# Kernel tuning notes

Hardware: AMD Instinct MI355X
Metric: run time of the kernel (lower is better)

Reference implementation:

```python
import jax, jax.numpy as jnp
import numpy as np

NUM_NODES = 100000
NUM_NEIGHS = 64
FEAT = 128
BATCH = 16384
NUM_SAMPLES = 16


def setup_inputs() -> dict:
    key = jax.random.key(0)
    k_ids, k_feat, k_adj = jax.random.split(key, 3)
    ids = jax.random.randint(k_ids, (BATCH,), 0, NUM_NODES, dtype=jnp.int64 if jax.config.jax_enable_x64 else jnp.int32)
    features = jax.random.normal(k_feat, (NUM_NODES, FEAT), dtype=jnp.float32)
    adj_info = jax.random.randint(k_adj, (NUM_NODES, NUM_NEIGHS), 0, NUM_NODES, dtype=jnp.int32)
    return {
        "ids": ids,
        "num_samples": NUM_SAMPLES,
        "features": features,
        "batch_size": BATCH,
        "adj_info": adj_info,
    }


def reference(ids, num_samples, features, batch_size, adj_info):
    # Gather adjacency rows and center-node features
    adj_lists = jnp.take(adj_info, ids, axis=0)            # [B, K]
    node_features = jnp.take(features, ids, axis=0)        # [B, F]
    neighbor_feature = jnp.take(features, adj_lists, axis=0)  # [B, K, F]
    # Euclidean distance center -> each neighbor (broadcast instead of tile)
    diff = node_features[:, None, :] - neighbor_feature    # [B, K, F]
    distance = jnp.sqrt(jnp.sum(diff * diff, axis=-1))     # [B, K]
    prob = jnp.exp(-distance)
    prob = prob / jnp.sum(prob, axis=-1, keepdims=True)    # [B, K]
    # Categorical sampling of num_samples neighbors per row
    logits = jnp.log(prob)
    skey = jax.random.key(42)
    samples_idx = jax.random.categorical(skey, logits, axis=-1, shape=(num_samples, batch_size)).T  # [B, S]
    selected = jnp.take_along_axis(adj_lists, samples_idx, axis=1)  # [B, S]
    return selected
```

## Files before the change

kernel.cpp:

```cpp
#include <hip/hip_runtime.h>
#include <stdint.h>

#define NB 16384
#define NK 64
#define NF 128
#define NS 16
#define RPB 4

__device__ __forceinline__ float xla_exp_f32(float x_in) {
#pragma clang fp contract(off)
  const float exp_hi = 88.3762626647950f;
  const float exp_lo = -88.3762626647949f;
  const float log2ef = 1.44269504088896341f;
  const float c1 = 0.693359375f;
  const float c2 = -2.12194440e-4f;
  const float p0 = 1.9875691500E-4f;
  const float p1 = 1.3981999507E-3f;
  const float p2 = 8.3334519073E-3f;
  const float p3 = 4.1665795894E-2f;
  const float p4 = 1.6666665459E-1f;
  const float p5 = 5.0000001201E-1f;

  float x = fminf(fmaxf(x_in, exp_lo), exp_hi);
  float fx = floorf(fmaf(x, log2ef, 0.5f));
  float tmp = c1 * fx;
  float z2 = c2 * fx;
  x = x - tmp;
  x = x - z2;
  float z = x * x;
  float y = fmaf(x, p0, p1);
  y = fmaf(y, x, p2);
  y = fmaf(y, x, p3);
  y = fmaf(y, x, p4);
  y = fmaf(y, x, p5);
  y = fmaf(y, z, x);
  y = y + 1.0f;
  int n = (int)fx;
  float two_n = __int_as_float((n + 127) << 23);
  return fmaxf(y * two_n, x_in);
}

__device__ __forceinline__ float xla_log_f32(float x_in) {
#pragma clang fp contract(off)
  const float sqrthf = 0.707106781186547524f;
  const float p0 = 7.0376836292E-2f;
  const float p1 = -1.1514610310E-1f;
  const float p2 = 1.1676998740E-1f;
  const float p3 = -1.2420140846E-1f;
  const float p4 = 1.4249322787E-1f;
  const float p5 = -1.6668057665E-1f;
  const float p6 = 2.0000714765E-1f;
  const float p7 = -2.4999993993E-1f;
  const float p8 = 3.3333331174E-1f;
  const float q1 = -2.12194440e-4f;
  const float q2 = 0.693359375f;

  float t = fmaxf(x_in, __uint_as_float(0x00800000u));
  uint32_t bits = __float_as_uint(t);
  float e = (float)((int)(bits >> 23) - 0x7f) + 1.0f;
  float m = __uint_as_float((bits & 0x007fffffu) | 0x3f000000u);
  bool lt = (m < sqrthf);
  float madd = lt ? m : 0.0f;
  e = e - (lt ? 1.0f : 0.0f);
  m = (m + madd) - 1.0f;

  float z = m * m;
  float y = fmaf(m, p0, p1);
  y = fmaf(y, m, p2);
  y = fmaf(y, m, p3);
  y = fmaf(y, m, p4);
  y = fmaf(y, m, p5);
  y = fmaf(y, m, p6);
  y = fmaf(y, m, p7);
  y = fmaf(y, m, p8);
  y = y * m;
  y = y * z;
  y = fmaf(e, q1, y);
  y = y - 0.5f * z;
  float r = m + y;
  r = fmaf(e, q2, r);
  return r;
}

__device__ __forceinline__ void threefry2x32_k42(uint32_t c0, uint32_t c1,
                                                 uint32_t& o0, uint32_t& o1) {
  const uint32_t k0 = 0u, k1 = 42u;
  const uint32_t k2 = k0 ^ k1 ^ 0x1BD11BDAu;
  uint32_t x0 = c0 + k0, x1 = c1 + k1;
#define TF_R(r) { x0 += x1; x1 = (x1 << (r)) | (x1 >> (32 - (r))); x1 ^= x0; }
  TF_R(13) TF_R(15) TF_R(26) TF_R(6)
  x0 += k1; x1 += k2 + 1u;
  TF_R(17) TF_R(29) TF_R(16) TF_R(24)
  x0 += k2; x1 += k0 + 2u;
  TF_R(13) TF_R(15) TF_R(26) TF_R(6)
  x0 += k0; x1 += k1 + 3u;
  TF_R(17) TF_R(29) TF_R(16) TF_R(24)
  x0 += k1; x1 += k2 + 4u;
  TF_R(13) TF_R(15) TF_R(26) TF_R(6)
  x0 += k2; x1 += k0 + 5u;
#undef TF_R
  o0 = x0; o1 = x1;
}

__device__ __forceinline__ uint32_t jax_random_bits32(uint32_t m) {
  uint32_t a, b;
  threefry2x32_k42(0u, m, a, b);
  return a ^ b;
}

__device__ __forceinline__ float gumbel_from_bits(uint32_t bits) {
#pragma clang fp contract(off)
  const float tiny = 1.17549435e-38f;
  float f = __uint_as_float((bits >> 9) | 0x3f800000u) - 1.0f;
  float u = fmaxf(tiny, f + tiny);
  return -xla_log_f32(-xla_log_f32(u));
}

#define AS1 __attribute__((address_space(1)))
#define AS3 __attribute__((address_space(3)))

__global__ void __launch_bounds__(256)
dns_kernel(const int* __restrict__ ids, const float* __restrict__ features,
           const int* __restrict__ adj, int* __restrict__ out) {
#pragma clang fp contract(off)
  __shared__ __align__(16) char sbuf[RPB][8192];
  __shared__ __align__(16) float fc[RPB][NF];
  __shared__ __align__(16) float esh[RPB][NK];
  __shared__ int nsh[RPB][NK];
  __shared__ float zb[RPB][NS][4];
  __shared__ int ib[RPB][NS][4];

  const int wave = threadIdx.x >> 6;
  const int k = threadIdx.x & 63;
  const int b = blockIdx.x * RPB + wave;
  char* sb = sbuf[wave];

  float pg[16];
#define GUM1(ss) pg[ss] = gumbel_from_bits(                                  \
      jax_random_bits32((uint32_t)(((ss) * NB + b) * NK + k)))

  const int center = ids[b];
  GUM1(0); GUM1(1); GUM1(2);

  if (k < NF / 4)
    ((float4*)fc[wave])[k] = ((const float4*)(features + (size_t)center * NF))[k];
  nsh[wave][k] = adj[(size_t)center * NK + k];

  GUM1(3); GUM1(4); GUM1(5);
  asm volatile("s_waitcnt lgkmcnt(0)" ::: "memory");

  const int rg = k >> 3;
  const int eg = k & 7;
  const int es = eg ^ rg;

  const float4* f4b = (const float4*)features;
#define MKGP(i) const float4* gp##i = f4b + (size_t)nsh[wave][(i) * 8 + rg] * (NF / 4) + es
  MKGP(0); MKGP(1); MKGP(2); MKGP(3); MKGP(4); MKGP(5); MKGP(6); MKGP(7);
#undef MKGP

#define STAGEQ()                                                             \
  do {                                                                       \
    __builtin_amdgcn_global_load_lds((const AS1 void*)gp0,                   \
        (AS3 void*)(sb + 0 * 1024), 16, 0, 0);                               \
    __builtin_amdgcn_global_load_lds((const AS1 void*)gp1,                   \
        (AS3 void*)(sb + 1 * 1024), 16, 0, 0);                               \
    __builtin_amdgcn_global_load_lds((const AS1 void*)gp2,                   \
        (AS3 void*)(sb + 2 * 1024), 16, 0, 0);                               \
    __builtin_amdgcn_global_load_lds((const AS1 void*)gp3,                   \
        (AS3 void*)(sb + 3 * 1024), 16, 0, 0);                               \
    __builtin_amdgcn_global_load_lds((const AS1 void*)gp4,                   \
        (AS3 void*)(sb + 4 * 1024), 16, 0, 0);                               \
    __builtin_amdgcn_global_load_lds((const AS1 void*)gp5,                   \
        (AS3 void*)(sb + 5 * 1024), 16, 0, 0);                               \
    __builtin_amdgcn_global_load_lds((const AS1 void*)gp6,                   \
        (AS3 void*)(sb + 6 * 1024), 16, 0, 0);                               \
    __builtin_amdgcn_global_load_lds((const AS1 void*)gp7,                   \
        (AS3 void*)(sb + 7 * 1024), 16, 0, 0);                               \
    gp0 += 8; gp1 += 8; gp2 += 8; gp3 += 8;                                  \
    gp4 += 8; gp5 += 8; gp6 += 8; gp7 += 8;                                  \
  } while (0)

#define CONSUMEQ(q)                                                          \
  do {                                                                       \
    _Pragma("unroll")                                                        \
    for (int j2 = 0; j2 < 8; ++j2) {                                         \
      const float4 v =                                                       \
          *(const float4*)(sb + k * 128 + ((j2 ^ (k & 7)) << 4));            \
      const int j = (q) * 8 + j2;                                            \
      float d0 = fc[wave][4 * j + 0] - v.x; acc = acc + d0 * d0;             \
      float d1 = fc[wave][4 * j + 1] - v.y; acc = acc + d1 * d1;             \
      float d2 = fc[wave][4 * j + 2] - v.z; acc = acc + d2 * d2;             \
      float d3 = fc[wave][4 * j + 3] - v.w; acc = acc + d3 * d3;             \
    }                                                                        \
  } while (0)

  float acc = 0.0f;

  STAGEQ(); GUM1(6); GUM1(7); GUM1(8);
  asm volatile("s_waitcnt vmcnt(0)" ::: "memory");
  CONSUMEQ(0);
  asm volatile("s_waitcnt lgkmcnt(0)" ::: "memory");

  STAGEQ(); GUM1(9); GUM1(10); GUM1(11);
  asm volatile("s_waitcnt vmcnt(0)" ::: "memory");
  CONSUMEQ(1);
  asm volatile("s_waitcnt lgkmcnt(0)" ::: "memory");

  STAGEQ(); GUM1(12); GUM1(13);
  asm volatile("s_waitcnt vmcnt(0)" ::: "memory");
  CONSUMEQ(2);
  asm volatile("s_waitcnt lgkmcnt(0)" ::: "memory");

  STAGEQ(); GUM1(14); GUM1(15);
  asm volatile("s_waitcnt vmcnt(0)" ::: "memory");
  CONSUMEQ(3);
  asm volatile("s_waitcnt lgkmcnt(0)" ::: "memory");

  const float ev = xla_exp_f32(-sqrtf(acc));
  esh[wave][k] = ev;
  asm volatile("s_waitcnt lgkmcnt(0)" ::: "memory");

  float s = 0.0f;
  const float4* e4 = (const float4*)esh[wave];
#pragma unroll
  for (int i = 0; i < NK / 4; ++i) {
    float4 v = e4[i];
    s = s + v.x; s = s + v.y; s = s + v.z; s = s + v.w;
  }
  const float logit = xla_log_f32(ev / s);

  float (*zsh)[NK + 1] = (float (*)[NK + 1])(void*)sb;
#pragma unroll
  for (int ss = 0; ss < NS; ++ss) {
    zsh[ss][k] = pg[ss] + logit;
  }
  asm volatile("s_waitcnt lgkmcnt(0)" ::: "memory");

  const int samp = k >> 2;
  const int sub = k & 3;
  const int kbase = sub * 16;
  float best = zsh[samp][kbase];
  int bi = kbase;
#pragma unroll 1
  for (int j = 1; j < 16; ++j) {
    const float v = zsh[samp][kbase + j];
    if (v > best) { best = v; bi = kbase + j; }
  }
  zb[wave][samp][sub] = best;
  ib[wave][samp][sub] = bi;
  asm volatile("s_waitcnt lgkmcnt(0)" ::: "memory");

  if (sub == 0) {
    float bb = zb[wave][samp][0];
    int bbi = ib[wave][samp][0];
#pragma unroll
    for (int qq = 1; qq < 4; ++qq) {
      const float v = zb[wave][samp][qq];
      if (v > bb) { bb = v; bbi = ib[wave][samp][qq]; }
    }
    out[b * NS + samp] = nsh[wave][bbi];
  }
#undef STAGEQ
#undef CONSUMEQ
#undef GUM1
}

extern "C" void kernel_launch(void* const* d_in, const int* in_sizes, int n_in,
                              void* d_out, int out_size, void* d_ws, size_t ws_size,
                              hipStream_t stream) {
  const int* ids = (const int*)d_in[0];
  const float* features = (const float*)d_in[2];
  const int* adj = (const int*)d_in[4];
  int* out = (int*)d_out;
  (void)in_sizes; (void)n_in; (void)out_size; (void)d_ws; (void)ws_size;

  dns_kernel<<<dim3(NB / RPB), dim3(64 * RPB), 0, stream>>>(ids, features, adj, out);
}
```

Before: 81.80 us.

## Split neighbor row loads between LDS staging and direct register loads to shrink LDS

Each lane now fetches half of each 32-float chunk of its own neighbor's feature row straight into registers. The other half still goes through global_load_lds staging into a smaller, re-swizzled LDS buffer. This cuts per-wave LDS from 8KB to 4.5KB, and launch bounds are raised to request 6 blocks per SM, so more waves can hide the gather latency. The cost is more register pressure from the held float4 values, and the direct loads are uncoalesced per-lane row accesses.

```diff
diff --git a/kernel.cpp b/kernel.cpp
--- a/kernel.cpp
+++ b/kernel.cpp
@@ -119,11 +119,11 @@
 #define AS1 __attribute__((address_space(1)))
 #define AS3 __attribute__((address_space(3)))
 
-__global__ void __launch_bounds__(256)
+__global__ void __launch_bounds__(256, 6)
 dns_kernel(const int* __restrict__ ids, const float* __restrict__ features,
            const int* __restrict__ adj, int* __restrict__ out) {
 #pragma clang fp contract(off)
-  __shared__ __align__(16) char sbuf[RPB][8192];
+  __shared__ __align__(16) char sbuf[RPB][4608];
   __shared__ __align__(16) float fc[RPB][NF];
   __shared__ __align__(16) float esh[RPB][NK];
   __shared__ int nsh[RPB][NK];
@@ -142,79 +142,83 @@
   const int center = ids[b];
   GUM1(0); GUM1(1); GUM1(2);
 
+  const int rn = adj[(size_t)center * NK + k];
+  nsh[wave][k] = rn;
   if (k < NF / 4)
     ((float4*)fc[wave])[k] = ((const float4*)(features + (size_t)center * NF))[k];
-  nsh[wave][k] = adj[(size_t)center * NK + k];
 
   GUM1(3); GUM1(4); GUM1(5);
   asm volatile("s_waitcnt lgkmcnt(0)" ::: "memory");
 
-  const int rg = k >> 3;
-  const int eg = k & 7;
-  const int es = eg ^ rg;
-
+  const int rsub = k >> 2;
+  const int gsw = (k & 3) ^ (rsub & 3);
   const float4* f4b = (const float4*)features;
-#define MKGP(i) const float4* gp##i = f4b + (size_t)nsh[wave][(i) * 8 + rg] * (NF / 4) + es
-  MKGP(0); MKGP(1); MKGP(2); MKGP(3); MKGP(4); MKGP(5); MKGP(6); MKGP(7);
-#undef MKGP
-
-#define STAGEQ()                                                             \
-  do {                                                                       \
-    __builtin_amdgcn_global_load_lds((const AS1 void*)gp0,                   \
+  const float4* gp0 = f4b + (size_t)nsh[wave][0 * 16 + rsub] * (NF / 4) + gsw;
+  const float4* gp1 = f4b + (size_t)nsh[wave][1 * 16 + rsub] * (NF / 4) + gsw;
+  const float4* gp2 = f4b + (size_t)nsh[wave][2 * 16 + rsub] * (NF / 4) + gsw;
+  const float4* gp3 = f4b + (size_t)nsh[wave][3 * 16 + rsub] * (NF / 4) + gsw;
+  const float4* gbase = f4b + (size_t)rn * (NF / 4);
+
+  const int csw = k & 3;
+  const char* crow = sb + k * 64;
+  const float4* fc4 = (const float4*)fc[wave];
+  float acc = 0.0f;
+
+#define STAGE_L(L)                                                           \
+    __builtin_amdgcn_global_load_lds((const AS1 void*)(gp0 + (L) * 8),       \
         (AS3 void*)(sb + 0 * 1024), 16, 0, 0);                               \
-    __builtin_amdgcn_global_load_lds((const AS1 void*)gp1,                   \
+    __builtin_amdgcn_global_load_lds((const AS1 void*)(gp1 + (L) * 8),       \
         (AS3 void*)(sb + 1 * 1024), 16, 0, 0);                               \
-    __builtin_amdgcn_global_load_lds((const AS1 void*)gp2,                   \
+    __builtin_amdgcn_global_load_lds((const AS1 void*)(gp2 + (L) * 8),       \
         (AS3 void*)(sb + 2 * 1024), 16, 0, 0);                               \
-    __builtin_amdgcn_global_load_lds((const AS1 void*)gp3,                   \
+    __builtin_amdgcn_global_load_lds((const AS1 void*)(gp3 + (L) * 8),       \
         (AS3 void*)(sb + 3 * 1024), 16, 0, 0);                               \
-    __builtin_amdgcn_global_load_lds((const AS1 void*)gp4,                   \
-        (AS3 void*)(sb + 4 * 1024), 16, 0, 0);                               \
-    __builtin_amdgcn_global_load_lds((const AS1 void*)gp5,                   \
-        (AS3 void*)(sb + 5 * 1024), 16, 0, 0);                               \
-    __builtin_amdgcn_global_load_lds((const AS1 void*)gp6,                   \
-        (AS3 void*)(sb + 6 * 1024), 16, 0, 0);                               \
-    __builtin_amdgcn_global_load_lds((const AS1 void*)gp7,                   \
-        (AS3 void*)(sb + 7 * 1024), 16, 0, 0);                               \
-    gp0 += 8; gp1 += 8; gp2 += 8; gp3 += 8;                                  \
-    gp4 += 8; gp5 += 8; gp6 += 8; gp7 += 8;                                  \
-  } while (0)
-
-#define CONSUMEQ(q)                                                          \
-  do {                                                                       \
+    const float4 sc0_##L = gbase[(L) * 8 + 4];                               \
+    const float4 sc1_##L = gbase[(L) * 8 + 5];                               \
+    const float4 sc2_##L = gbase[(L) * 8 + 6];                               \
+    const float4 sc3_##L = gbase[(L) * 8 + 7]
+
+#define DQ(f, v)                                                             \
+    { float d0 = (f).x - (v).x; acc = acc + d0 * d0;                         \
+      float d1 = (f).y - (v).y; acc = acc + d1 * d1;                         \
+      float d2 = (f).z - (v).z; acc = acc + d2 * d2;                         \
+      float d3 = (f).w - (v).w; acc = acc + d3 * d3; }
+
+#define CONSUME_L(L)                                                         \
     _Pragma("unroll")                                                        \
-    for (int j2 = 0; j2 < 8; ++j2) {                                         \
-      const float4 v =                                                       \
-          *(const float4*)(sb + k * 128 + ((j2 ^ (k & 7)) << 4));            \
-      const int j = (q) * 8 + j2;                                            \
-      float d0 = fc[wave][4 * j + 0] - v.x; acc = acc + d0 * d0;             \
-      float d1 = fc[wave][4 * j + 1] - v.y; acc = acc + d1 * d1;             \
-      float d2 = fc[wave][4 * j + 2] - v.z; acc = acc + d2 * d2;             \
-      float d3 = fc[wave][4 * j + 3] - v.w; acc = acc + d3 * d3;             \
+    for (int t = 0; t < 4; ++t) {                                            \
+      const float4 v = *(const float4*)(crow + ((t ^ csw) << 4));            \
+      DQ(fc4[(L) * 8 + t], v);                                               \
     }                                                                        \
-  } while (0)
-
-  float acc = 0.0f;
-
-  STAGEQ(); GUM1(6); GUM1(7); GUM1(8);
-  asm volatile("s_waitcnt vmcnt(0)" ::: "memory");
-  CONSUMEQ(0);
-  asm volatile("s_waitcnt lgkmcnt(0)" ::: "memory");
-
-  STAGEQ(); GUM1(9); GUM1(10); GUM1(11);
-  asm volatile("s_waitcnt vmcnt(0)" ::: "memory");
-  CONSUMEQ(1);
-  asm volatile("s_waitcnt lgkmcnt(0)" ::: "memory");
-
-  STAGEQ(); GUM1(12); GUM1(13);
-  asm volatile("s_waitcnt vmcnt(0)" ::: "memory");
-  CONSUMEQ(2);
-  asm volatile("s_waitcnt lgkmcnt(0)" ::: "memory");
-
-  STAGEQ(); GUM1(14); GUM1(15);
-  asm volatile("s_waitcnt vmcnt(0)" ::: "memory");
-  CONSUMEQ(3);
-  asm volatile("s_waitcnt lgkmcnt(0)" ::: "memory");
+    DQ(fc4[(L) * 8 + 4], sc0_##L);                                           \
+    DQ(fc4[(L) * 8 + 5], sc1_##L);                                           \
+    DQ(fc4[(L) * 8 + 6], sc2_##L);                                           \
+    DQ(fc4[(L) * 8 + 7], sc3_##L)
+
+  {
+    STAGE_L(0); GUM1(6); GUM1(7); GUM1(8);
+    asm volatile("s_waitcnt vmcnt(0)" ::: "memory");
+    CONSUME_L(0);
+    asm volatile("s_waitcnt lgkmcnt(0)" ::: "memory");
+  }
+  {
+    STAGE_L(1); GUM1(9); GUM1(10); GUM1(11);
+    asm volatile("s_waitcnt vmcnt(0)" ::: "memory");
+    CONSUME_L(1);
+    asm volatile("s_waitcnt lgkmcnt(0)" ::: "memory");
+  }
+  {
+    STAGE_L(2); GUM1(12); GUM1(13);
+    asm volatile("s_waitcnt vmcnt(0)" ::: "memory");
+    CONSUME_L(2);
+    asm volatile("s_waitcnt lgkmcnt(0)" ::: "memory");
+  }
+  {
+    STAGE_L(3); GUM1(14); GUM1(15);
+    asm volatile("s_waitcnt vmcnt(0)" ::: "memory");
+    CONSUME_L(3);
+    asm volatile("s_waitcnt lgkmcnt(0)" ::: "memory");
+  }
 
   const float ev = xla_exp_f32(-sqrtf(acc));
   esh[wave][k] = ev;
@@ -260,8 +264,9 @@
     }
     out[b * NS + samp] = nsh[wave][bbi];
   }
-#undef STAGEQ
-#undef CONSUMEQ
+#undef STAGE_L
+#undef CONSUME_L
+#undef DQ
 #undef GUM1
 }
 
```

Result: slower. 84.36 us (median of 2 runs) (+3.1%).
